# Kernel optimization log

Hardware: AMD Instinct MI355X
Metric: run time of the kernel (lower is better)

Reference implementation:

```python
import jax, jax.numpy as jnp
import numpy as np

NQ = 12  # num_qubits
NL = 4   # num_layers (StronglyEntanglingLayers depth)
BATCH = 512


def _rx(a):
    # RX(a) = [[cos(a/2), -i sin(a/2)], [-i sin(a/2), cos(a/2)]]; a: (...,) float -> (...,2,2) complex64
    c = jnp.cos(a / 2)
    s = jnp.sin(a / 2)
    return jnp.stack([jnp.stack([c + 0j, -1j * s], -1),
                      jnp.stack([-1j * s, c + 0j], -1)], -2)


def _rot(phi, theta, omega):
    # Pennylane Rot(phi,theta,omega) = RZ(omega) RY(theta) RZ(phi)
    ct = jnp.cos(theta / 2)
    st = jnp.sin(theta / 2)
    ep = jnp.exp(-0.5j * (phi + omega))   # e^{-i(phi+omega)/2}
    em = jnp.exp(-0.5j * (phi - omega))   # e^{-i(phi-omega)/2}
    return jnp.stack([jnp.stack([ep * ct, -jnp.conj(em) * st], -1),
                      jnp.stack([em * st, jnp.conj(ep) * ct], -1)], -2)


def _apply_1q_shared(state, U, q):
    # state: (B,) + (2,)*n; U: (2,2) shared across batch
    s = jnp.moveaxis(state, q + 1, -1)
    s = s @ U.T
    return jnp.moveaxis(s, -1, q + 1)


def _apply_1q_batched(state, U, q):
    # U: (B,2,2), one gate per batch element (AngleEmbedding)
    s = jnp.moveaxis(state, q + 1, -1)
    s = jnp.einsum('b...i,bij->b...j', s, U)
    return jnp.moveaxis(s, -1, q + 1)


def _apply_cnot(state, c, t):
    # flip target axis on the control=1 slice
    s = jnp.moveaxis(state, (c + 1, t + 1), (1, 2))  # (B,2,2,rest)
    s = jnp.stack([s[:, 0], s[:, 1, ::-1]], axis=1)
    return jnp.moveaxis(s, (1, 2), (c + 1, t + 1))


def _circuit(batch_inputs, weights):
    B, n = batch_inputs.shape
    state = jnp.zeros((B, 2 ** n), jnp.complex64).at[:, 0].set(1.0)
    state = state.reshape((B,) + (2,) * n)
    # AngleEmbedding: RX(x_i) on wire i
    Ux = _rx(batch_inputs)  # (B,n,2,2)
    for q in range(n):
        state = _apply_1q_batched(state, Ux[:, q], q)
    # StronglyEntanglingLayers: per layer Rot on each wire then CNOT ring with range r
    Ur = _rot(weights[..., 0], weights[..., 1], weights[..., 2])  # (L,n,2,2)
    for l in range(NL):
        for q in range(n):
            state = _apply_1q_shared(state, Ur[l, q], q)
        r = (l % (n - 1)) + 1  # pennylane default ranges
        for q in range(n):
            state = _apply_cnot(state, q, (q + r) % n)
    # <Z_q> = p(0 on q) - p(1 on q)
    probs = state.real ** 2 + state.imag ** 2
    zs = []
    for q in range(n):
        p = jnp.moveaxis(probs, q + 1, 1).reshape(B, 2, -1).sum(-1)
        zs.append(p[:, 0] - p[:, 1])
    return jnp.stack(zs, axis=1)  # (B,n) float32


def setup_inputs() -> dict:
    key = jax.random.key(0)
    k1, k2, k3, k4 = jax.random.split(key, 4)
    return {
        'batch_inputs': jax.random.normal(k1, (BATCH, NQ), dtype=jnp.float32),
        'weights': jax.random.normal(k2, (NL, NQ, 3), dtype=jnp.float32),
        'head_w': jax.random.normal(k3, (1, NQ), dtype=jnp.float32) / np.sqrt(NQ),
        'head_b': jax.random.normal(k4, (1,), dtype=jnp.float32),
    }


def reference(batch_inputs, weights, head_w, head_b):
    expvals = _circuit(batch_inputs, weights)      # (B, NQ)
    return (expvals @ head_w.T + head_b)[:, 0]     # (B,)
```

## Files before the change

kernel.cpp:

```cpp
#include <hip/hip_runtime.h>

#define NQ 12
#define NL 4
#define NT 256

typedef float f32x2 __attribute__((ext_vector_type(2)));

constexpr unsigned sidx_c(unsigned x) { return x ^ ((x >> 4) & 15u) ^ ((x >> 8) & 15u); }

constexpr unsigned gmap_inv(int l, unsigned v) {
    int r = l + 1; unsigned x = v;
    for (int q = 0; q < NQ; ++q) {
        int cb = NQ - 1 - q, tw = (q + r) % NQ, tb = NQ - 1 - tw;
        x ^= ((x >> cb) & 1u) << tb;
    }
    return x;
}

struct Tabs {
    unsigned lcol[NL][8];
    unsigned scol[NL][16];
};
constexpr Tabs make_tabs() {
    Tabs T{};
    for (int l = 0; l < NL; ++l) {
        unsigned colb[12];
        for (int bit = 0; bit < 12; ++bit) colb[bit] = sidx_c(gmap_inv(l, 1u << bit)) << 3;
        for (int j = 0; j < 6; ++j) T.lcol[l][j] = colb[4 + j];
        T.lcol[l][6] = colb[10];
        T.lcol[l][7] = colb[11];
        for (int s = 0; s < 16; ++s) {
            unsigned v = 0;
            for (int bp = 0; bp < 4; ++bp) if ((s >> bp) & 1) v ^= colb[bp];
            T.scol[l][s] = v;
        }
    }
    return T;
}
__constant__ Tabs TB = make_tabs();

__device__ __forceinline__ unsigned dsidx(unsigned x) { return x ^ ((x >> 4) & 15u) ^ ((x >> 8) & 15u); }

template<int IMM>
__device__ __forceinline__ f32x2 swz2(f32x2 v) {
    f32x2 r;
    r.x = __int_as_float(__builtin_amdgcn_ds_swizzle(__float_as_int(v.x), IMM));
    r.y = __int_as_float(__builtin_amdgcn_ds_swizzle(__float_as_int(v.y), IMM));
    return r;
}
template<int CTRL>
__device__ __forceinline__ f32x2 dpp2(f32x2 v) {
    f32x2 r;
    r.x = __int_as_float(__builtin_amdgcn_update_dpp(__float_as_int(v.x), __float_as_int(v.x), CTRL, 0xF, 0xF, false));
    r.y = __int_as_float(__builtin_amdgcn_update_dpp(__float_as_int(v.y), __float_as_int(v.y), CTRL, 0xF, 0xF, false));
    return r;
}
__device__ __forceinline__ f32x2 shfl2(f32x2 v, int m) {
    f32x2 r; r.x = __shfl_xor(v.x, m, 64); r.y = __shfl_xor(v.y, m, 64); return r;
}

__global__ __launch_bounds__(NT) void qsim_kernel(
    const float* __restrict__ xin,
    const float* __restrict__ wts,
    const float* __restrict__ hw,
    const float* __restrict__ hb,
    float* __restrict__ out)
{
    __shared__ float2 stbuf[2][4096];
    __shared__ float  gm[NL * NQ][8];
    __shared__ float  wred[4];

    const int tid  = threadIdx.x;
    const int lane = tid & 63;
    const int wv   = tid >> 6;
    const int b    = blockIdx.x;

    if (tid < NL * NQ) {
        const float phi = wts[tid * 3 + 0];
        const float th  = wts[tid * 3 + 1];
        const float om  = wts[tid * 3 + 2];
        const float ct  = cosf(0.5f * th), stt = sinf(0.5f * th);
        const float apo = -0.5f * (phi + om), amo = -0.5f * (phi - om);
        const float epr = cosf(apo), epi = sinf(apo);
        const float emr = cosf(amo), emi = sinf(amo);
        float* g = gm[tid];
        g[0] =  epr * ct;  g[1] =  epi * ct;
        g[2] = -emr * stt; g[3] =  emi * stt;
        g[4] =  emr * stt; g[5] =  emi * stt;
        g[6] =  epr * ct;  g[7] = -epi * ct;
    }

    float cv[NQ], sv[NQ];
    #pragma unroll
    for (int bp = 0; bp < NQ; ++bp) {
        const float a = 0.5f * xin[b * NQ + (NQ - 1 - bp)];
        cv[bp] = cosf(a); sv[bp] = sinf(a);
    }

    const unsigned xbase = ((unsigned)wv << 10) | ((unsigned)lane << 4);
    const unsigned wbyte = dsidx(xbase) << 3;

    {
        float MLW = 1.f;
        #pragma unroll
        for (int j = 0; j < 6; ++j) MLW *= ((lane >> j) & 1) ? sv[4 + j] : cv[4 + j];
        MLW *= (wv & 1) ? sv[10] : cv[10];
        MLW *= (wv >> 1) ? sv[11] : cv[11];
        const int pcLW = (__popc((unsigned)lane) + __popc((unsigned)wv)) & 3;
        const float plr = (pcLW == 0) ? 1.f : ((pcLW == 2) ? -1.f : 0.f);
        const float pli = (pcLW == 1) ? -1.f : ((pcLW == 3) ? 1.f : 0.f);
        float MS[16];
        MS[0] = cv[0]; MS[1] = sv[0];
        #pragma unroll
        for (int bit = 1; bit < 4; ++bit) {
            #pragma unroll
            for (int j = (1 << bit) - 1; j >= 0; --j) {
                MS[j | (1 << bit)] = MS[j] * sv[bit];
                MS[j]              = MS[j] * cv[bit];
            }
        }
        #pragma unroll
        for (int s = 0; s < 16; ++s) {
            const float m = MLW * MS[s];
            const int pcS = __builtin_popcount((unsigned)s) & 3;
            float ar, ai;
            if      (pcS == 0) { ar =  m * plr; ai =  m * pli; }
            else if (pcS == 1) { ar =  m * pli; ai = -m * plr; }
            else if (pcS == 2) { ar = -m * plr; ai = -m * pli; }
            else               { ar = -m * pli; ai =  m * plr; }
            *(float2*)((char*)stbuf[0] + (wbyte ^ ((unsigned)s << 3))) = make_float2(ar, ai);
        }
    }
    __syncthreads();

    f32x2 rp[8], ip[8];
    const int b11 = wv >> 1, b10 = wv & 1;

    for (int l = 0; l < NL; ++l) {
        const float2* rb = stbuf[l & 1];
        float2*       wb = stbuf[(l + 1) & 1];

        {
            const float4 ga0 = *(const float4*)(&gm[l * NQ + 0][0]);
            const float4 gb0 = *(const float4*)(&gm[l * NQ + 0][4]);
            const float4 ga1 = *(const float4*)(&gm[l * NQ + 1][0]);
            const float4 gb1 = *(const float4*)(&gm[l * NQ + 1][4]);
            const float d0r = b11 ? gb0.z : ga0.x, d0i = b11 ? gb0.w : ga0.y;
            const float o0r = b11 ? gb0.x : ga0.z, o0i = b11 ? gb0.y : ga0.w;
            const float d1r = b10 ? gb1.z : ga1.x, d1i = b10 ? gb1.w : ga1.y;
            const float o1r = b10 ? gb1.x : ga1.z, o1i = b10 ? gb1.y : ga1.w;
            const float dwr  = d0r * d1r - d0i * d1i, dwi  = d0r * d1i + d0i * d1r;
            const float dp1r = o0r * d1r - o0i * d1i, dp1i = o0r * d1i + o0i * d1r;
            const float dp2r = d0r * o1r - d0i * o1i, dp2i = d0r * o1i + d0i * o1r;
            const float dp3r = o0r * o1r - o0i * o1i, dp3i = o0r * o1i + o0i * o1r;
            #pragma unroll
            for (int k = 0; k < 8; ++k) {
                const unsigned a0 = wbyte ^ ((unsigned)(2 * k) << 3);
                const unsigned a1 = a0 ^ 8u;
                const float2 o_0 = *(const float2*)((const char*)rb + a0);
                const float2 o_1 = *(const float2*)((const char*)rb + a1);
                const float2 u_0 = *(const float2*)((const char*)rb + (a0 ^ 0x4040u));
                const float2 u_1 = *(const float2*)((const char*)rb + (a1 ^ 0x4040u));
                const float2 v_0 = *(const float2*)((const char*)rb + (a0 ^ 0x2020u));
                const float2 v_1 = *(const float2*)((const char*)rb + (a1 ^ 0x2020u));
                const float2 w_0 = *(const float2*)((const char*)rb + (a0 ^ 0x6060u));
                const float2 w_1 = *(const float2*)((const char*)rb + (a1 ^ 0x6060u));
                const f32x2 orr = f32x2{o_0.x, o_1.x}, oii = f32x2{o_0.y, o_1.y};
                const f32x2 p1r = f32x2{u_0.x, u_1.x}, p1i = f32x2{u_0.y, u_1.y};
                const f32x2 p2r = f32x2{v_0.x, v_1.x}, p2i = f32x2{v_0.y, v_1.y};
                const f32x2 p3r = f32x2{w_0.x, w_1.x}, p3i = f32x2{w_0.y, w_1.y};
                rp[k] = dwr*orr - dwi*oii + dp1r*p1r - dp1i*p1i + dp2r*p2r - dp2i*p2i + dp3r*p3r - dp3i*p3i;
                ip[k] = dwi*orr + dwr*oii + dp1i*p1r + dp1r*p1i + dp2i*p2r + dp2r*p2i + dp3i*p3r + dp3r*p3i;
            }
        }

        {
            const float4 ga = *(const float4*)(&gm[l * NQ + 2][0]);
            const float4 gb_ = *(const float4*)(&gm[l * NQ + 2][4]);
            const int lb = (lane >> 5) & 1;
            const float cMer = lb ? gb_.z : ga.x, cMei = lb ? gb_.w : ga.y;
            const float cOtr = lb ? gb_.x : ga.z, cOti = lb ? gb_.y : ga.w;
            #pragma unroll
            for (int k = 0; k < 8; ++k) {
                const f32x2 pR = shfl2(rp[k], 32), pI = shfl2(ip[k], 32);
                const f32x2 nr = cMer*rp[k] - cMei*ip[k] + cOtr*pR - cOti*pI;
                const f32x2 ni = cMei*rp[k] + cMer*ip[k] + cOti*pR + cOtr*pI;
                rp[k] = nr; ip[k] = ni;
            }
        }
        {
            const float4 ga = *(const float4*)(&gm[l * NQ + 3][0]);
            const float4 gb_ = *(const float4*)(&gm[l * NQ + 3][4]);
            const int lb = (lane >> 4) & 1;
            const float cMer = lb ? gb_.z : ga.x, cMei = lb ? gb_.w : ga.y;
            const float cOtr = lb ? gb_.x : ga.z, cOti = lb ? gb_.y : ga.w;
            #pragma unroll
            for (int k = 0; k < 8; ++k) {
                const f32x2 pR = swz2<0x401F>(rp[k]), pI = swz2<0x401F>(ip[k]);
                const f32x2 nr = cMer*rp[k] - cMei*ip[k] + cOtr*pR - cOti*pI;
                const f32x2 ni = cMei*rp[k] + cMer*ip[k] + cOti*pR + cOtr*pI;
                rp[k] = nr; ip[k] = ni;
            }
        }
        {
            const float4 ga = *(const float4*)(&gm[l * NQ + 4][0]);
            const float4 gb_ = *(const float4*)(&gm[l * NQ + 4][4]);
            const int lb = (lane >> 3) & 1;
            const float cMer = lb ? gb_.z : ga.x, cMei = lb ? gb_.w : ga.y;
            const float cOtr = lb ? gb_.x : ga.z, cOti = lb ? gb_.y : ga.w;
            #pragma unroll
            for (int k = 0; k < 8; ++k) {
                const f32x2 pR = swz2<0x201F>(rp[k]), pI = swz2<0x201F>(ip[k]);
                const f32x2 nr = cMer*rp[k] - cMei*ip[k] + cOtr*pR - cOti*pI;
                const f32x2 ni = cMei*rp[k] + cMer*ip[k] + cOti*pR + cOtr*pI;
                rp[k] = nr; ip[k] = ni;
            }
        }
        {
            const float4 ga = *(const float4*)(&gm[l * NQ + 5][0]);
            const float4 gb_ = *(const float4*)(&gm[l * NQ + 5][4]);
            const int lb = (lane >> 2) & 1;
            const float cMer = lb ? gb_.z : ga.x, cMei = lb ? gb_.w : ga.y;
            const float cOtr = lb ? gb_.x : ga.z, cOti = lb ? gb_.y : ga.w;
            #pragma unroll
            for (int k = 0; k < 8; ++k) {
                const f32x2 pR = swz2<0x101F>(rp[k]), pI = swz2<0x101F>(ip[k]);
                const f32x2 nr = cMer*rp[k] - cMei*ip[k] + cOtr*pR - cOti*pI;
                const f32x2 ni = cMei*rp[k] + cMer*ip[k] + cOti*pR + cOtr*pI;
                rp[k] = nr; ip[k] = ni;
            }
        }
        {
            const float4 ga = *(const float4*)(&gm[l * NQ + 6][0]);
            const float4 gb_ = *(const float4*)(&gm[l * NQ + 6][4]);
            const int lb = (lane >> 1) & 1;
            const float cMer = lb ? gb_.z : ga.x, cMei = lb ? gb_.w : ga.y;
            const float cOtr = lb ? gb_.x : ga.z, cOti = lb ? gb_.y : ga.w;
            #pragma unroll
            for (int k = 0; k < 8; ++k) {
                const f32x2 pR = dpp2<0x4E>(rp[k]), pI = dpp2<0x4E>(ip[k]);
                const f32x2 nr = cMer*rp[k] - cMei*ip[k] + cOtr*pR - cOti*pI;
                const f32x2 ni = cMei*rp[k] + cMer*ip[k] + cOti*pR + cOtr*pI;
                rp[k] = nr; ip[k] = ni;
            }
        }
        {
            const float4 ga = *(const float4*)(&gm[l * NQ + 7][0]);
            const float4 gb_ = *(const float4*)(&gm[l * NQ + 7][4]);
            const int lb = lane & 1;
            const float cMer = lb ? gb_.z : ga.x, cMei = lb ? gb_.w : ga.y;
            const float cOtr = lb ? gb_.x : ga.z, cOti = lb ? gb_.y : ga.w;
            #pragma unroll
            for (int k = 0; k < 8; ++k) {
                const f32x2 pR = dpp2<0xB1>(rp[k]), pI = dpp2<0xB1>(ip[k]);
                const f32x2 nr = cMer*rp[k] - cMei*ip[k] + cOtr*pR - cOti*pI;
                const f32x2 ni = cMei*rp[k] + cMer*ip[k] + cOti*pR + cOtr*pI;
                rp[k] = nr; ip[k] = ni;
            }
        }
        #pragma unroll
        for (int wq = 8; wq <= 10; ++wq) {
            const int rb2 = 10 - wq;
            const float4 ga = *(const float4*)(&gm[l * NQ + wq][0]);
            const float4 gb_ = *(const float4*)(&gm[l * NQ + wq][4]);
            #pragma unroll
            for (int h = 0; h < 4; ++h) {
                const int k0 = ((h >> rb2) << (rb2 + 1)) | (h & ((1 << rb2) - 1));
                const int k1 = k0 | (1 << rb2);
                const f32x2 a0r = rp[k0], a0i = ip[k0], a1r = rp[k1], a1i = ip[k1];
                rp[k0] = ga.x*a0r - ga.y*a0i + ga.z*a1r - ga.w*a1i;
                ip[k0] = ga.y*a0r + ga.x*a0i + ga.w*a1r + ga.z*a1i;
                rp[k1] = gb_.x*a0r - gb_.y*a0i + gb_.z*a1r - gb_.w*a1i;
                ip[k1] = gb_.y*a0r + gb_.x*a0i + gb_.w*a1r + gb_.z*a1i;
            }
        }
        {
            const float4 ga = *(const float4*)(&gm[l * NQ + 11][0]);
            const float4 gb_ = *(const float4*)(&gm[l * NQ + 11][4]);
            #pragma unroll
            for (int k = 0; k < 8; ++k) {
                const float a0r = rp[k].x, a0i = ip[k].x, a1r = rp[k].y, a1i = ip[k].y;
                rp[k].x = ga.x*a0r - ga.y*a0i + ga.z*a1r - ga.w*a1i;
                ip[k].x = ga.y*a0r + ga.x*a0i + ga.w*a1r + ga.z*a1i;
                rp[k].y = gb_.x*a0r - gb_.y*a0i + gb_.z*a1r - gb_.w*a1i;
                ip[k].y = gb_.y*a0r + gb_.x*a0i + gb_.w*a1r + gb_.z*a1i;
            }
        }

        {
            unsigned sbase = 0;
            #pragma unroll
            for (int j = 0; j < 6; ++j) if ((lane >> j) & 1) sbase ^= TB.lcol[l][j];
            if (b10) sbase ^= TB.lcol[l][6];
            if (b11) sbase ^= TB.lcol[l][7];
            #pragma unroll
            for (int k = 0; k < 8; ++k) {
                *(float2*)((char*)wb + (sbase ^ TB.scol[l][2 * k]))     = make_float2(rp[k].x, ip[k].x);
                *(float2*)((char*)wb + (sbase ^ TB.scol[l][2 * k + 1])) = make_float2(rp[k].y, ip[k].y);
            }
        }
        __syncthreads();
    }

    {
        float CS[16];
        CS[0] = hw[11]; CS[1] = -hw[11];
        #pragma unroll
        for (int bit = 1; bit < 4; ++bit) {
            const float h = hw[11 - bit];
            #pragma unroll
            for (int j = (1 << bit) - 1; j >= 0; --j) {
                CS[j | (1 << bit)] = CS[j] - h;
                CS[j]              = CS[j] + h;
            }
        }
        float CW = b11 ? -hw[0] : hw[0];
        CW += b10 ? -hw[1] : hw[1];
        #pragma unroll
        for (int q = 2; q <= 7; ++q)
            CW += ((lane >> (7 - q)) & 1) ? -hw[q] : hw[q];

        f32x2 acc = f32x2{0.f, 0.f};
        #pragma unroll
        for (int k = 0; k < 8; ++k) {
            const unsigned a0 = wbyte ^ ((unsigned)(2 * k) << 3);
            const float2 v0 = *(const float2*)((const char*)stbuf[0] + a0);
            const float2 v1 = *(const float2*)((const char*)stbuf[0] + (a0 ^ 8u));
            const f32x2 vr = f32x2{v0.x, v1.x}, vi = f32x2{v0.y, v1.y};
            const f32x2 pr = vr * vr + vi * vi;
            acc += pr * f32x2{CW + CS[2 * k], CW + CS[2 * k + 1]};
        }
        float sres = acc.x + acc.y;
        #pragma unroll
        for (int off = 32; off >= 1; off >>= 1)
            sres += __shfl_xor(sres, off, 64);
        if ((tid & 63) == 0) wred[wv] = sres;
        __syncthreads();
        if (tid == 0) out[b] = wred[0] + wred[1] + wred[2] + wred[3] + hb[0];
    }
}

extern "C" void kernel_launch(void* const* d_in, const int* in_sizes, int n_in,
                              void* d_out, int out_size, void* d_ws, size_t ws_size,
                              hipStream_t stream) {
    const float* x  = (const float*)d_in[0];
    const float* wt = (const float*)d_in[1];
    const float* hw = (const float*)d_in[2];
    const float* hb = (const float*)d_in[3];
    float* outp = (float*)d_out;
    const int B = in_sizes[0] / NQ;
    qsim_kernel<<<B, NT, 0, stream>>>(x, wt, hw, hb, outp);
}
```

Before: 35.01 us.

## Fold first-layer gates into init, skip final scatter, use permlane swaps

The layer-0 gates on wires 0 and 1 are applied analytically to the product-state initialisation in registers, so the initial LDS write and read go away. The last layer's CNOT permutation is absorbed into precomputed parity masks for the Z-expectation weights, which removes the final scatter and reload. Cross-lane exchanges for wires 2 and 3 now use permlane32/16 swaps instead of shfl and ds_swizzle, and fast __sinf/__cosf replace the precise versions. The state buffer is single-buffered, which needs an extra barrier per layer.

```diff
diff --git a/kernel.cpp b/kernel.cpp
--- a/kernel.cpp
+++ b/kernel.cpp
@@ -18,12 +18,13 @@
 }
 
 struct Tabs {
-    unsigned lcol[NL][8];
-    unsigned scol[NL][16];
+    unsigned lcol[3][8];
+    unsigned scol[3][16];
+    unsigned rfin[NQ];
 };
 constexpr Tabs make_tabs() {
     Tabs T{};
-    for (int l = 0; l < NL; ++l) {
+    for (int l = 0; l < 3; ++l) {
         unsigned colb[12];
         for (int bit = 0; bit < 12; ++bit) colb[bit] = sidx_c(gmap_inv(l, 1u << bit)) << 3;
         for (int j = 0; j < 6; ++j) T.lcol[l][j] = colb[4 + j];
@@ -35,19 +36,18 @@
             T.scol[l][s] = v;
         }
     }
+    for (int q = 0; q < NQ; ++q) {
+        const int bpos = 11 - q;
+        unsigned m = 0;
+        for (int j = 0; j < 12; ++j)
+            m |= ((gmap_inv(3, 1u << j) >> bpos) & 1u) << j;
+        T.rfin[q] = m;
+    }
     return T;
 }
 __constant__ Tabs TB = make_tabs();
-
-__device__ __forceinline__ unsigned dsidx(unsigned x) { return x ^ ((x >> 4) & 15u) ^ ((x >> 8) & 15u); }
-
-template<int IMM>
-__device__ __forceinline__ f32x2 swz2(f32x2 v) {
-    f32x2 r;
-    r.x = __int_as_float(__builtin_amdgcn_ds_swizzle(__float_as_int(v.x), IMM));
-    r.y = __int_as_float(__builtin_amdgcn_ds_swizzle(__float_as_int(v.y), IMM));
-    return r;
-}
+constexpr Tabs CT = make_tabs();
+
 template<int CTRL>
 __device__ __forceinline__ f32x2 dpp2(f32x2 v) {
     f32x2 r;
@@ -55,8 +55,186 @@
     r.y = __int_as_float(__builtin_amdgcn_update_dpp(__float_as_int(v.y), __float_as_int(v.y), CTRL, 0xF, 0xF, false));
     return r;
 }
-__device__ __forceinline__ f32x2 shfl2(f32x2 v, int m) {
-    f32x2 r; r.x = __shfl_xor(v.x, m, 64); r.y = __shfl_xor(v.y, m, 64); return r;
+__device__ __forceinline__ void pswap32(f32x2 v, f32x2& lo, f32x2& hi) {
+    float ax = v.x, bx = v.x;
+    asm("v_permlane32_swap_b32 %0, %1" : "+v"(ax), "+v"(bx));
+    float ay = v.y, by = v.y;
+    asm("v_permlane32_swap_b32 %0, %1" : "+v"(ay), "+v"(by));
+    lo = f32x2{ax, ay}; hi = f32x2{bx, by};
+}
+__device__ __forceinline__ void pswap16(f32x2 v, f32x2& ev, f32x2& od) {
+    float ax = v.x, bx = v.x;
+    asm("v_permlane16_swap_b32 %0, %1" : "+v"(ax), "+v"(bx));
+    float ay = v.y, by = v.y;
+    asm("v_permlane16_swap_b32 %0, %1" : "+v"(ay), "+v"(by));
+    ev = f32x2{ax, ay}; od = f32x2{bx, by};
+}
+
+__device__ __forceinline__ void gates2to11(f32x2 rp[8], f32x2 ip[8], const float (*gmL)[8], int lane) {
+    {
+        const float4 ga = *(const float4*)&gmL[2][0];
+        const float4 gb = *(const float4*)&gmL[2][4];
+        const int h = (lane >> 5) & 1;
+        const float car = h ? gb.x : ga.x, cai = h ? gb.y : ga.y;
+        const float cbr = h ? gb.z : ga.z, cbi = h ? gb.w : ga.w;
+        #pragma unroll
+        for (int k = 0; k < 8; ++k) {
+            f32x2 r0r, r1r, r0i, r1i;
+            pswap32(rp[k], r0r, r1r);
+            pswap32(ip[k], r0i, r1i);
+            rp[k] = car*r0r - cai*r0i + cbr*r1r - cbi*r1i;
+            ip[k] = cai*r0r + car*r0i + cbi*r1r + cbr*r1i;
+        }
+    }
+    {
+        const float4 ga = *(const float4*)&gmL[3][0];
+        const float4 gb = *(const float4*)&gmL[3][4];
+        const int h = (lane >> 4) & 1;
+        const float car = h ? gb.x : ga.x, cai = h ? gb.y : ga.y;
+        const float cbr = h ? gb.z : ga.z, cbi = h ? gb.w : ga.w;
+        #pragma unroll
+        for (int k = 0; k < 8; ++k) {
+            f32x2 r0r, r1r, r0i, r1i;
+            pswap16(rp[k], r0r, r1r);
+            pswap16(ip[k], r0i, r1i);
+            rp[k] = car*r0r - cai*r0i + cbr*r1r - cbi*r1i;
+            ip[k] = cai*r0r + car*r0i + cbi*r1r + cbr*r1i;
+        }
+    }
+    {
+        const float4 ga = *(const float4*)&gmL[4][0];
+        const float4 gb = *(const float4*)&gmL[4][4];
+        const int h = (lane >> 3) & 1;
+        const float cMer = h ? gb.z : ga.x, cMei = h ? gb.w : ga.y;
+        const float cOtr = h ? gb.x : ga.z, cOti = h ? gb.y : ga.w;
+        #pragma unroll
+        for (int k = 0; k < 8; ++k) {
+            const f32x2 pR = dpp2<0x128>(rp[k]), pI = dpp2<0x128>(ip[k]);
+            const f32x2 nr = cMer*rp[k] - cMei*ip[k] + cOtr*pR - cOti*pI;
+            const f32x2 ni = cMei*rp[k] + cMer*ip[k] + cOti*pR + cOtr*pI;
+            rp[k] = nr; ip[k] = ni;
+        }
+    }
+    {
+        const float4 ga = *(const float4*)&gmL[5][0];
+        const float4 gb = *(const float4*)&gmL[5][4];
+        const int h = (lane >> 2) & 1;
+        const float cMer = h ? gb.z : ga.x, cMei = h ? gb.w : ga.y;
+        const float cOtr = h ? gb.x : ga.z, cOti = h ? gb.y : ga.w;
+        #pragma unroll
+        for (int k = 0; k < 8; ++k) {
+            const f32x2 pR = dpp2<0xB1>(dpp2<0x4E>(dpp2<0x141>(rp[k])));
+            const f32x2 pI = dpp2<0xB1>(dpp2<0x4E>(dpp2<0x141>(ip[k])));
+            const f32x2 nr = cMer*rp[k] - cMei*ip[k] + cOtr*pR - cOti*pI;
+            const f32x2 ni = cMei*rp[k] + cMer*ip[k] + cOti*pR + cOtr*pI;
+            rp[k] = nr; ip[k] = ni;
+        }
+    }
+    {
+        const float4 ga = *(const float4*)&gmL[6][0];
+        const float4 gb = *(const float4*)&gmL[6][4];
+        const int h = (lane >> 1) & 1;
+        const float cMer = h ? gb.z : ga.x, cMei = h ? gb.w : ga.y;
+        const float cOtr = h ? gb.x : ga.z, cOti = h ? gb.y : ga.w;
+        #pragma unroll
+        for (int k = 0; k < 8; ++k) {
+            const f32x2 pR = dpp2<0x4E>(rp[k]), pI = dpp2<0x4E>(ip[k]);
+            const f32x2 nr = cMer*rp[k] - cMei*ip[k] + cOtr*pR - cOti*pI;
+            const f32x2 ni = cMei*rp[k] + cMer*ip[k] + cOti*pR + cOtr*pI;
+            rp[k] = nr; ip[k] = ni;
+        }
+    }
+    {
+        const float4 ga = *(const float4*)&gmL[7][0];
+        const float4 gb = *(const float4*)&gmL[7][4];
+        const int h = lane & 1;
+        const float cMer = h ? gb.z : ga.x, cMei = h ? gb.w : ga.y;
+        const float cOtr = h ? gb.x : ga.z, cOti = h ? gb.y : ga.w;
+        #pragma unroll
+        for (int k = 0; k < 8; ++k) {
+            const f32x2 pR = dpp2<0xB1>(rp[k]), pI = dpp2<0xB1>(ip[k]);
+            const f32x2 nr = cMer*rp[k] - cMei*ip[k] + cOtr*pR - cOti*pI;
+            const f32x2 ni = cMei*rp[k] + cMer*ip[k] + cOti*pR + cOtr*pI;
+            rp[k] = nr; ip[k] = ni;
+        }
+    }
+    #pragma unroll
+    for (int wq = 8; wq <= 10; ++wq) {
+        const int rb2 = 10 - wq;
+        const float4 ga = *(const float4*)&gmL[wq][0];
+        const float4 gb = *(const float4*)&gmL[wq][4];
+        #pragma unroll
+        for (int h2 = 0; h2 < 4; ++h2) {
+            const int k0 = ((h2 >> rb2) << (rb2 + 1)) | (h2 & ((1 << rb2) - 1));
+            const int k1 = k0 | (1 << rb2);
+            const f32x2 a0r = rp[k0], a0i = ip[k0], a1r = rp[k1], a1i = ip[k1];
+            rp[k0] = ga.x*a0r - ga.y*a0i + ga.z*a1r - ga.w*a1i;
+            ip[k0] = ga.y*a0r + ga.x*a0i + ga.w*a1r + ga.z*a1i;
+            rp[k1] = gb.x*a0r - gb.y*a0i + gb.z*a1r - gb.w*a1i;
+            ip[k1] = gb.y*a0r + gb.x*a0i + gb.w*a1r + gb.z*a1i;
+        }
+    }
+    {
+        const float4 ga = *(const float4*)&gmL[11][0];
+        const float4 gb = *(const float4*)&gmL[11][4];
+        const f32x2 K0r = f32x2{ga.x, gb.x}, K0i = f32x2{ga.y, gb.y};
+        const f32x2 K1r = f32x2{ga.z, gb.z}, K1i = f32x2{ga.w, gb.w};
+        #pragma unroll
+        for (int k = 0; k < 8; ++k) {
+            const float a0r = rp[k].x, a0i = ip[k].x, a1r = rp[k].y, a1i = ip[k].y;
+            rp[k] = K0r*a0r - K0i*a0i + K1r*a1r - K1i*a1i;
+            ip[k] = K0i*a0r + K0r*a0i + K1i*a1r + K1r*a1i;
+        }
+    }
+}
+
+__device__ __forceinline__ void read_w01(f32x2 rp[8], f32x2 ip[8], const float2* st, unsigned wbyte,
+                                         const float (*gmL)[8], int b11, int b10) {
+    const float4 ga0 = *(const float4*)&gmL[0][0];
+    const float4 gb0 = *(const float4*)&gmL[0][4];
+    const float4 ga1 = *(const float4*)&gmL[1][0];
+    const float4 gb1 = *(const float4*)&gmL[1][4];
+    const float d0r = b11 ? gb0.z : ga0.x, d0i = b11 ? gb0.w : ga0.y;
+    const float o0r = b11 ? gb0.x : ga0.z, o0i = b11 ? gb0.y : ga0.w;
+    const float d1r = b10 ? gb1.z : ga1.x, d1i = b10 ? gb1.w : ga1.y;
+    const float o1r = b10 ? gb1.x : ga1.z, o1i = b10 ? gb1.y : ga1.w;
+    const float dwr  = d0r*d1r - d0i*d1i, dwi  = d0r*d1i + d0i*d1r;
+    const float dp1r = o0r*d1r - o0i*d1i, dp1i = o0r*d1i + o0i*d1r;
+    const float dp2r = d0r*o1r - d0i*o1i, dp2i = d0r*o1i + d0i*o1r;
+    const float dp3r = o0r*o1r - o0i*o1i, dp3i = o0r*o1i + o0i*o1r;
+    #pragma unroll
+    for (int k = 0; k < 8; ++k) {
+        const unsigned a0 = wbyte ^ ((unsigned)(2 * k) << 3);
+        const unsigned a1 = a0 ^ 8u;
+        const float2 o_0 = *(const float2*)((const char*)st + a0);
+        const float2 o_1 = *(const float2*)((const char*)st + a1);
+        const float2 v_0 = *(const float2*)((const char*)st + (a0 ^ 0x2020u));
+        const float2 v_1 = *(const float2*)((const char*)st + (a1 ^ 0x2020u));
+        const float2 u_0 = *(const float2*)((const char*)st + (a0 ^ 0x4040u));
+        const float2 u_1 = *(const float2*)((const char*)st + (a1 ^ 0x4040u));
+        const float2 w_0 = *(const float2*)((const char*)st + (a0 ^ 0x6060u));
+        const float2 w_1 = *(const float2*)((const char*)st + (a1 ^ 0x6060u));
+        const f32x2 orr = f32x2{o_0.x, o_1.x}, oii = f32x2{o_0.y, o_1.y};
+        const f32x2 p2r = f32x2{v_0.x, v_1.x}, p2i = f32x2{v_0.y, v_1.y};
+        const f32x2 p1r = f32x2{u_0.x, u_1.x}, p1i = f32x2{u_0.y, u_1.y};
+        const f32x2 p3r = f32x2{w_0.x, w_1.x}, p3i = f32x2{w_0.y, w_1.y};
+        rp[k] = dwr*orr - dwi*oii + dp1r*p1r - dp1i*p1i + dp2r*p2r - dp2i*p2i + dp3r*p3r - dp3i*p3i;
+        ip[k] = dwi*orr + dwr*oii + dp1i*p1r + dp1r*p1i + dp2i*p2r + dp2r*p2i + dp3i*p3r + dp3r*p3i;
+    }
+}
+
+__device__ __forceinline__ void scatter_l(const f32x2 rp[8], const f32x2 ip[8], float2* st,
+                                          int l, int lane, int b10, int b11) {
+    unsigned sbase = 0;
+    #pragma unroll
+    for (int j = 0; j < 6; ++j) if ((lane >> j) & 1) sbase ^= TB.lcol[l][j];
+    if (b10) sbase ^= TB.lcol[l][6];
+    if (b11) sbase ^= TB.lcol[l][7];
+    #pragma unroll
+    for (int k = 0; k < 8; ++k) {
+        *(float2*)((char*)st + (sbase ^ TB.scol[l][2 * k]))     = make_float2(rp[k].x, ip[k].x);
+        *(float2*)((char*)st + (sbase ^ TB.scol[l][2 * k + 1])) = make_float2(rp[k].y, ip[k].y);
+    }
 }
 
 __global__ __launch_bounds__(NT) void qsim_kernel(
@@ -66,7 +244,7 @@
     const float* __restrict__ hb,
     float* __restrict__ out)
 {
-    __shared__ float2 stbuf[2][4096];
+    __shared__ float2 st[4096];
     __shared__ float  gm[NL * NQ][8];
     __shared__ float  wred[4];
 
@@ -74,6 +252,7 @@
     const int lane = tid & 63;
     const int wv   = tid >> 6;
     const int b    = blockIdx.x;
+    const int b11  = wv >> 1, b10 = wv & 1;
 
     if (tid < NL * NQ) {
         const float phi = wts[tid * 3 + 0];
@@ -94,241 +273,95 @@
     #pragma unroll
     for (int bp = 0; bp < NQ; ++bp) {
         const float a = 0.5f * xin[b * NQ + (NQ - 1 - bp)];
-        cv[bp] = cosf(a); sv[bp] = sinf(a);
+        cv[bp] = __cosf(a); sv[bp] = __sinf(a);
+    }
+    float MS[16];
+    MS[0] = cv[0]; MS[1] = sv[0];
+    #pragma unroll
+    for (int bit = 1; bit < 4; ++bit) {
+        #pragma unroll
+        for (int j = (1 << bit) - 1; j >= 0; --j) {
+            MS[j | (1 << bit)] = MS[j] * sv[bit];
+            MS[j]              = MS[j] * cv[bit];
+        }
     }
 
     const unsigned xbase = ((unsigned)wv << 10) | ((unsigned)lane << 4);
-    const unsigned wbyte = dsidx(xbase) << 3;
-
-    {
-        float MLW = 1.f;
-        #pragma unroll
-        for (int j = 0; j < 6; ++j) MLW *= ((lane >> j) & 1) ? sv[4 + j] : cv[4 + j];
-        MLW *= (wv & 1) ? sv[10] : cv[10];
-        MLW *= (wv >> 1) ? sv[11] : cv[11];
-        const int pcLW = (__popc((unsigned)lane) + __popc((unsigned)wv)) & 3;
-        const float plr = (pcLW == 0) ? 1.f : ((pcLW == 2) ? -1.f : 0.f);
-        const float pli = (pcLW == 1) ? -1.f : ((pcLW == 3) ? 1.f : 0.f);
-        float MS[16];
-        MS[0] = cv[0]; MS[1] = sv[0];
-        #pragma unroll
-        for (int bit = 1; bit < 4; ++bit) {
+    const unsigned wbyte = (xbase ^ ((xbase >> 4) & 15u) ^ ((xbase >> 8) & 15u)) << 3;
+
+    __syncthreads();
+
+    f32x2 rp[8], ip[8];
+
+    {
+        const float m00 = cv[11]*cv[10], m01 = cv[11]*sv[10];
+        const float m10 = sv[11]*cv[10], m11s = sv[11]*sv[10];
+        const float* G0 = gm[0];
+        const float* G1 = gm[1];
+        const float u0ar = b11 ? G0[4] : G0[0], u0ai = b11 ? G0[5] : G0[1];
+        const float u0br = b11 ? G0[6] : G0[2], u0bi = b11 ? G0[7] : G0[3];
+        const float u1ar = b10 ? G1[4] : G1[0], u1ai = b10 ? G1[5] : G1[1];
+        const float u1br = b10 ? G1[6] : G1[2], u1bi = b10 ? G1[7] : G1[3];
+        const float t0r = u0ar*m00 + u0bi*m10;
+        const float t0i = u0ai*m00 - u0br*m10;
+        const float t1r = u0ai*m01 - u0br*m11s;
+        const float t1i = -(u0ar*m01) - u0bi*m11s;
+        float Ar = u1ar*t0r - u1ai*t0i + u1br*t1r - u1bi*t1i;
+        float Ai = u1ai*t0r + u1ar*t0i + u1bi*t1r + u1br*t1i;
+        float mm = 1.f;
+        #pragma unroll
+        for (int j = 0; j < 6; ++j) mm *= ((lane >> j) & 1) ? sv[4 + j] : cv[4 + j];
+        Ar *= mm; Ai *= mm;
+        const int pcl = __popc((unsigned)lane) & 3;
+        float Br, Bi;
+        if      (pcl == 0) { Br =  Ar; Bi =  Ai; }
+        else if (pcl == 1) { Br =  Ai; Bi = -Ar; }
+        else if (pcl == 2) { Br = -Ar; Bi = -Ai; }
+        else               { Br = -Ai; Bi =  Ar; }
+        #pragma unroll
+        for (int s = 0; s < 16; ++s) {
+            const float m = MS[s];
+            const int pc = __builtin_popcount((unsigned)s) & 3;
+            float ar, ai;
+            if      (pc == 0) { ar =  Br*m; ai =  Bi*m; }
+            else if (pc == 1) { ar =  Bi*m; ai = -Br*m; }
+            else if (pc == 2) { ar = -Br*m; ai = -Bi*m; }
+            else              { ar = -Bi*m; ai =  Br*m; }
+            if (s & 1) { rp[s >> 1].y = ar; ip[s >> 1].y = ai; }
+            else       { rp[s >> 1].x = ar; ip[s >> 1].x = ai; }
+        }
+        gates2to11(rp, ip, &gm[0], lane);
+        scatter_l(rp, ip, st, 0, lane, b10, b11);
+    }
+    __syncthreads();
+
+    for (int l = 1; l < NL; ++l) {
+        read_w01(rp, ip, st, wbyte, &gm[l * NQ], b11, b10);
+        gates2to11(rp, ip, &gm[l * NQ], lane);
+        if (l < 3) {
+            __syncthreads();
+            scatter_l(rp, ip, st, l, lane, b10, b11);
+            __syncthreads();
+        }
+    }
+
+    {
+        float CS[16];
+        #pragma unroll
+        for (int s = 0; s < 16; ++s) CS[s] = 0.f;
+        #pragma unroll
+        for (int q = 0; q < NQ; ++q) {
+            const unsigned m = CT.rfin[q];
+            const float wq = (__popc(xbase & m) & 1) ? -hw[q] : hw[q];
             #pragma unroll
-            for (int j = (1 << bit) - 1; j >= 0; --j) {
-                MS[j | (1 << bit)] = MS[j] * sv[bit];
-                MS[j]              = MS[j] * cv[bit];
-            }
-        }
-        #pragma unroll
-        for (int s = 0; s < 16; ++s) {
-            const float m = MLW * MS[s];
-            const int pcS = __builtin_popcount((unsigned)s) & 3;
-            float ar, ai;
-            if      (pcS == 0) { ar =  m * plr; ai =  m * pli; }
-            else if (pcS == 1) { ar =  m * pli; ai = -m * plr; }
-            else if (pcS == 2) { ar = -m * plr; ai = -m * pli; }
-            else               { ar = -m * pli; ai =  m * plr; }
-            *(float2*)((char*)stbuf[0] + (wbyte ^ ((unsigned)s << 3))) = make_float2(ar, ai);
-        }
-    }
-    __syncthreads();
-
-    f32x2 rp[8], ip[8];
-    const int b11 = wv >> 1, b10 = wv & 1;
-
-    for (int l = 0; l < NL; ++l) {
-        const float2* rb = stbuf[l & 1];
-        float2*       wb = stbuf[(l + 1) & 1];
-
-        {
-            const float4 ga0 = *(const float4*)(&gm[l * NQ + 0][0]);
-            const float4 gb0 = *(const float4*)(&gm[l * NQ + 0][4]);
-            const float4 ga1 = *(const float4*)(&gm[l * NQ + 1][0]);
-            const float4 gb1 = *(const float4*)(&gm[l * NQ + 1][4]);
-            const float d0r = b11 ? gb0.z : ga0.x, d0i = b11 ? gb0.w : ga0.y;
-            const float o0r = b11 ? gb0.x : ga0.z, o0i = b11 ? gb0.y : ga0.w;
-            const float d1r = b10 ? gb1.z : ga1.x, d1i = b10 ? gb1.w : ga1.y;
-            const float o1r = b10 ? gb1.x : ga1.z, o1i = b10 ? gb1.y : ga1.w;
-            const float dwr  = d0r * d1r - d0i * d1i, dwi  = d0r * d1i + d0i * d1r;
-            const float dp1r = o0r * d1r - o0i * d1i, dp1i = o0r * d1i + o0i * d1r;
-            const float dp2r = d0r * o1r - d0i * o1i, dp2i = d0r * o1i + d0i * o1r;
-            const float dp3r = o0r * o1r - o0i * o1i, dp3i = o0r * o1i + o0i * o1r;
-            #pragma unroll
-            for (int k = 0; k < 8; ++k) {
-                const unsigned a0 = wbyte ^ ((unsigned)(2 * k) << 3);
-                const unsigned a1 = a0 ^ 8u;
-                const float2 o_0 = *(const float2*)((const char*)rb + a0);
-                const float2 o_1 = *(const float2*)((const char*)rb + a1);
-                const float2 u_0 = *(const float2*)((const char*)rb + (a0 ^ 0x4040u));
-                const float2 u_1 = *(const float2*)((const char*)rb + (a1 ^ 0x4040u));
-                const float2 v_0 = *(const float2*)((const char*)rb + (a0 ^ 0x2020u));
-                const float2 v_1 = *(const float2*)((const char*)rb + (a1 ^ 0x2020u));
-                const float2 w_0 = *(const float2*)((const char*)rb + (a0 ^ 0x6060u));
-                const float2 w_1 = *(const float2*)((const char*)rb + (a1 ^ 0x6060u));
-                const f32x2 orr = f32x2{o_0.x, o_1.x}, oii = f32x2{o_0.y, o_1.y};
-                const f32x2 p1r = f32x2{u_0.x, u_1.x}, p1i = f32x2{u_0.y, u_1.y};
-                const f32x2 p2r = f32x2{v_0.x, v_1.x}, p2i = f32x2{v_0.y, v_1.y};
-                const f32x2 p3r = f32x2{w_0.x, w_1.x}, p3i = f32x2{w_0.y, w_1.y};
-                rp[k] = dwr*orr - dwi*oii + dp1r*p1r - dp1i*p1i + dp2r*p2r - dp2i*p2i + dp3r*p3r - dp3i*p3i;
-                ip[k] = dwi*orr + dwr*oii + dp1i*p1r + dp1r*p1i + dp2i*p2r + dp2r*p2i + dp3i*p3r + dp3r*p3i;
-            }
-        }
-
-        {
-            const float4 ga = *(const float4*)(&gm[l * NQ + 2][0]);
-            const float4 gb_ = *(const float4*)(&gm[l * NQ + 2][4]);
-            const int lb = (lane >> 5) & 1;
-            const float cMer = lb ? gb_.z : ga.x, cMei = lb ? gb_.w : ga.y;
-            const float cOtr = lb ? gb_.x : ga.z, cOti = lb ? gb_.y : ga.w;
-            #pragma unroll
-            for (int k = 0; k < 8; ++k) {
-                const f32x2 pR = shfl2(rp[k], 32), pI = shfl2(ip[k], 32);
-                const f32x2 nr = cMer*rp[k] - cMei*ip[k] + cOtr*pR - cOti*pI;
-                const f32x2 ni = cMei*rp[k] + cMer*ip[k] + cOti*pR + cOtr*pI;
-                rp[k] = nr; ip[k] = ni;
-            }
-        }
-        {
-            const float4 ga = *(const float4*)(&gm[l * NQ + 3][0]);
-            const float4 gb_ = *(const float4*)(&gm[l * NQ + 3][4]);
-            const int lb = (lane >> 4) & 1;
-            const float cMer = lb ? gb_.z : ga.x, cMei = lb ? gb_.w : ga.y;
-            const float cOtr = lb ? gb_.x : ga.z, cOti = lb ? gb_.y : ga.w;
-            #pragma unroll
-            for (int k = 0; k < 8; ++k) {
-                const f32x2 pR = swz2<0x401F>(rp[k]), pI = swz2<0x401F>(ip[k]);
-                const f32x2 nr = cMer*rp[k] - cMei*ip[k] + cOtr*pR - cOti*pI;
-                const f32x2 ni = cMei*rp[k] + cMer*ip[k] + cOti*pR + cOtr*pI;
-                rp[k] = nr; ip[k] = ni;
-            }
-        }
-        {
-            const float4 ga = *(const float4*)(&gm[l * NQ + 4][0]);
-            const float4 gb_ = *(const float4*)(&gm[l * NQ + 4][4]);
-            const int lb = (lane >> 3) & 1;
-            const float cMer = lb ? gb_.z : ga.x, cMei = lb ? gb_.w : ga.y;
-            const float cOtr = lb ? gb_.x : ga.z, cOti = lb ? gb_.y : ga.w;
-            #pragma unroll
-            for (int k = 0; k < 8; ++k) {
-                const f32x2 pR = swz2<0x201F>(rp[k]), pI = swz2<0x201F>(ip[k]);
-                const f32x2 nr = cMer*rp[k] - cMei*ip[k] + cOtr*pR - cOti*pI;
-                const f32x2 ni = cMei*rp[k] + cMer*ip[k] + cOti*pR + cOtr*pI;
-                rp[k] = nr; ip[k] = ni;
-            }
-        }
-        {
-            const float4 ga = *(const float4*)(&gm[l * NQ + 5][0]);
-            const float4 gb_ = *(const float4*)(&gm[l * NQ + 5][4]);
-            const int lb = (lane >> 2) & 1;
-            const float cMer = lb ? gb_.z : ga.x, cMei = lb ? gb_.w : ga.y;
-            const float cOtr = lb ? gb_.x : ga.z, cOti = lb ? gb_.y : ga.w;
-            #pragma unroll
-            for (int k = 0; k < 8; ++k) {
-                const f32x2 pR = swz2<0x101F>(rp[k]), pI = swz2<0x101F>(ip[k]);
-                const f32x2 nr = cMer*rp[k] - cMei*ip[k] + cOtr*pR - cOti*pI;
-                const f32x2 ni = cMei*rp[k] + cMer*ip[k] + cOti*pR + cOtr*pI;
-                rp[k] = nr; ip[k] = ni;
-            }
-        }
-        {
-            const float4 ga = *(const float4*)(&gm[l * NQ + 6][0]);
-            const float4 gb_ = *(const float4*)(&gm[l * NQ + 6][4]);
-            const int lb = (lane >> 1) & 1;
-            const float cMer = lb ? gb_.z : ga.x, cMei = lb ? gb_.w : ga.y;
-            const float cOtr = lb ? gb_.x : ga.z, cOti = lb ? gb_.y : ga.w;
-            #pragma unroll
-            for (int k = 0; k < 8; ++k) {
-                const f32x2 pR = dpp2<0x4E>(rp[k]), pI = dpp2<0x4E>(ip[k]);
-                const f32x2 nr = cMer*rp[k] - cMei*ip[k] + cOtr*pR - cOti*pI;
-                const f32x2 ni = cMei*rp[k] + cMer*ip[k] + cOti*pR + cOtr*pI;
-                rp[k] = nr; ip[k] = ni;
-            }
-        }
-        {
-            const float4 ga = *(const float4*)(&gm[l * NQ + 7][0]);
-            const float4 gb_ = *(const float4*)(&gm[l * NQ + 7][4]);
-            const int lb = lane & 1;
-            const float cMer = lb ? gb_.z : ga.x, cMei = lb ? gb_.w : ga.y;
-            const float cOtr = lb ? gb_.x : ga.z, cOti = lb ? gb_.y : ga.w;
-            #pragma unroll
-            for (int k = 0; k < 8; ++k) {
-                const f32x2 pR = dpp2<0xB1>(rp[k]), pI = dpp2<0xB1>(ip[k]);
-                const f32x2 nr = cMer*rp[k] - cMei*ip[k] + cOtr*pR - cOti*pI;
-                const f32x2 ni = cMei*rp[k] + cMer*ip[k] + cOti*pR + cOtr*pI;
-                rp[k] = nr; ip[k] = ni;
-            }
-        }
-        #pragma unroll
-        for (int wq = 8; wq <= 10; ++wq) {
-            const int rb2 = 10 - wq;
-            const float4 ga = *(const float4*)(&gm[l * NQ + wq][0]);
-            const float4 gb_ = *(const float4*)(&gm[l * NQ + wq][4]);
-            #pragma unroll
-            for (int h = 0; h < 4; ++h) {
-                const int k0 = ((h >> rb2) << (rb2 + 1)) | (h & ((1 << rb2) - 1));
-                const int k1 = k0 | (1 << rb2);
-                const f32x2 a0r = rp[k0], a0i = ip[k0], a1r = rp[k1], a1i = ip[k1];
-                rp[k0] = ga.x*a0r - ga.y*a0i + ga.z*a1r - ga.w*a1i;
-                ip[k0] = ga.y*a0r + ga.x*a0i + ga.w*a1r + ga.z*a1i;
-                rp[k1] = gb_.x*a0r - gb_.y*a0i + gb_.z*a1r - gb_.w*a1i;
-                ip[k1] = gb_.y*a0r + gb_.x*a0i + gb_.w*a1r + gb_.z*a1i;
-            }
-        }
-        {
-            const float4 ga = *(const float4*)(&gm[l * NQ + 11][0]);
-            const float4 gb_ = *(const float4*)(&gm[l * NQ + 11][4]);
-            #pragma unroll
-            for (int k = 0; k < 8; ++k) {
-                const float a0r = rp[k].x, a0i = ip[k].x, a1r = rp[k].y, a1i = ip[k].y;
-                rp[k].x = ga.x*a0r - ga.y*a0i + ga.z*a1r - ga.w*a1i;
-                ip[k].x = ga.y*a0r + ga.x*a0i + ga.w*a1r + ga.z*a1i;
-                rp[k].y = gb_.x*a0r - gb_.y*a0i + gb_.z*a1r - gb_.w*a1i;
-                ip[k].y = gb_.y*a0r + gb_.x*a0i + gb_.w*a1r + gb_.z*a1i;
-            }
-        }
-
-        {
-            unsigned sbase = 0;
-            #pragma unroll
-            for (int j = 0; j < 6; ++j) if ((lane >> j) & 1) sbase ^= TB.lcol[l][j];
-            if (b10) sbase ^= TB.lcol[l][6];
-            if (b11) sbase ^= TB.lcol[l][7];
-            #pragma unroll
-            for (int k = 0; k < 8; ++k) {
-                *(float2*)((char*)wb + (sbase ^ TB.scol[l][2 * k]))     = make_float2(rp[k].x, ip[k].x);
-                *(float2*)((char*)wb + (sbase ^ TB.scol[l][2 * k + 1])) = make_float2(rp[k].y, ip[k].y);
-            }
-        }
-        __syncthreads();
-    }
-
-    {
-        float CS[16];
-        CS[0] = hw[11]; CS[1] = -hw[11];
-        #pragma unroll
-        for (int bit = 1; bit < 4; ++bit) {
-            const float h = hw[11 - bit];
-            #pragma unroll
-            for (int j = (1 << bit) - 1; j >= 0; --j) {
-                CS[j | (1 << bit)] = CS[j] - h;
-                CS[j]              = CS[j] + h;
-            }
-        }
-        float CW = b11 ? -hw[0] : hw[0];
-        CW += b10 ? -hw[1] : hw[1];
-        #pragma unroll
-        for (int q = 2; q <= 7; ++q)
-            CW += ((lane >> (7 - q)) & 1) ? -hw[q] : hw[q];
-
+            for (int s = 0; s < 16; ++s)
+                CS[s] += (__builtin_popcount((unsigned)s & m) & 1) ? -wq : wq;
+        }
         f32x2 acc = f32x2{0.f, 0.f};
         #pragma unroll
         for (int k = 0; k < 8; ++k) {
-            const unsigned a0 = wbyte ^ ((unsigned)(2 * k) << 3);
-            const float2 v0 = *(const float2*)((const char*)stbuf[0] + a0);
-            const float2 v1 = *(const float2*)((const char*)stbuf[0] + (a0 ^ 8u));
-            const f32x2 vr = f32x2{v0.x, v1.x}, vi = f32x2{v0.y, v1.y};
-            const f32x2 pr = vr * vr + vi * vi;
-            acc += pr * f32x2{CW + CS[2 * k], CW + CS[2 * k + 1]};
+            const f32x2 pr = rp[k]*rp[k] + ip[k]*ip[k];
+            acc += pr * f32x2{CS[2 * k], CS[2 * k + 1]};
         }
         float sres = acc.x + acc.y;
         #pragma unroll
```

New measurement: 32.55 us. -7.0%, faster.
